# Optimization experiments

Measured on AMD Instinct MI355X. Metric: run time of the kernel, lower is better.

The kernel has to match this reference:

```python
import jax, jax.numpy as jnp
import numpy as np

B, Q, HID = 8, 8, 4096
H, KVH, D = 32, 8, 128
KV = 4096
ROPE_THETA = 10000.0


def rotate_half(x):
    x1, x2 = jnp.split(x, 2, axis=-1)
    return jnp.concatenate([-x2, x1], axis=-1)


def setup_inputs() -> dict:
    key = jax.random.key(0)
    ks = jax.random.split(key, 6)
    hidden_states = jax.random.normal(ks[0], (B, Q, HID), dtype=jnp.float32)
    position_ids = jnp.broadcast_to(jnp.arange(KV, dtype=jnp.int64), (B, KV))
    key_cache = jax.random.normal(ks[1], (B, KVH, KV, D), dtype=jnp.float32)
    value_cache = jax.random.normal(ks[2], (B, KVH, KV, D), dtype=jnp.float32)
    # mask: True -> blocked (-10000). Queries occupy last Q positions, causal.
    qpos = KV - Q + jnp.arange(Q)
    attention_mask = (jnp.arange(KV)[None, :] > qpos[:, None])[None, None]  # [1,1,Q,KV]
    attention_mask = jnp.broadcast_to(attention_mask, (B, 1, Q, KV))
    q_w = jax.random.normal(ks[3], (HID, HID), dtype=jnp.float32) * 0.02
    o_w = jax.random.normal(ks[4], (HID, HID), dtype=jnp.float32) * 0.02
    return {"hidden_states": hidden_states, "position_ids": position_ids,
            "key_cache": key_cache, "value_cache": value_cache,
            "attention_mask": attention_mask, "q_w": q_w, "o_w": o_w}


def reference(hidden_states, position_ids, key_cache, value_cache, attention_mask, q_w, o_w):
    # q projection: nn.Linear -> x @ W^T
    q = hidden_states @ q_w.T                       # [B,Q,HID]
    q = q.reshape(B, Q, H, D).transpose(0, 2, 1, 3)  # [B,H,Q,D]

    # rotary tables for kv_seq_len positions
    half = D // 2
    inv_freq = 1.0 / (ROPE_THETA ** (jnp.arange(0, half, dtype=jnp.float32) / half))
    t = jnp.arange(KV, dtype=jnp.float32)
    freqs = t[:, None] * inv_freq[None, :]           # [KV, D/2]
    emb = jnp.concatenate([freqs, freqs], axis=-1)   # [KV, D]
    cos_t, sin_t = jnp.cos(emb), jnp.sin(emb)

    # position_idx trick from the module: single effective rope position
    idx = jnp.argmax(position_ids.astype(jnp.int32), axis=1)[0]
    pid = jnp.take(position_ids, idx[None], axis=1)  # [B,1]
    cos = cos_t[pid][:, None]                        # [B,1,1,D]
    sin = sin_t[pid][:, None]
    q = q * cos + rotate_half(q) * sin               # [B,H,Q,D]

    # GQA attention without materializing repeat_kv (same math)
    G = H // KVH
    qg = q.reshape(B, KVH, G, Q, D)
    scores = jnp.einsum('bkgqd,bksd->bkgqs', qg, key_cache) / jnp.sqrt(jnp.float32(D))
    mask = attention_mask[:, :, None]                # [B,1,1,Q,KV]
    scores = jnp.where(mask, jnp.float32(-10000.0), scores)
    probs = jax.nn.softmax(scores.astype(jnp.float32), axis=-1).astype(q.dtype)
    out = jnp.einsum('bkgqs,bksd->bkgqd', probs, value_cache)  # [B,KVH,G,Q,D]
    out = out.reshape(B, H, Q, D).transpose(0, 2, 1, 3).reshape(B, Q, HID)
    return out @ o_w.T
```

## Files before the change

kernel.cpp:

```cpp
#include <hip/hip_runtime.h>
#include <math.h>

#define B_   8
#define Q_   8
#define HID  4096
#define NH   32
#define KVH_ 8
#define GQ   4
#define D_   128
#define KV_  4096
#define M_   64

#define OFF_COS   0
#define OFF_SIN   512
#define OFF_QROPE 1024
#define OFF_ATT   (OFF_QROPE + M_*HID)
#define OFF_OPART (OFF_ATT + M_*HID)
#define OFF_MPART (OFF_OPART + 64*8*32*128)
#define OFF_LPART (OFF_MPART + 64*8*32)
#define OFF_GPART (OFF_LPART + 64*8*32)

__global__ void prep_kernel(const int* __restrict__ pos, float* __restrict__ ws) {
    __shared__ int sv[256], si[256];
    __shared__ int s_idx;
    int t = threadIdx.x;
    int bv = -2147483647 - 1, bi = 0x7fffffff;
    for (int i = t; i < KV_; i += 256) {
        int v = pos[i];
        if (v > bv || (v == bv && i < bi)) { bv = v; bi = i; }
    }
    sv[t] = bv; si[t] = bi;
    __syncthreads();
    for (int off = 128; off > 0; off >>= 1) {
        if (t < off) {
            int v2 = sv[t + off], i2 = si[t + off];
            if (v2 > sv[t] || (v2 == sv[t] && i2 < si[t])) { sv[t] = v2; si[t] = i2; }
        }
        __syncthreads();
    }
    if (t == 0) s_idx = si[0];
    __syncthreads();
    int idx = s_idx;
    for (int u = t; u < B_ * 64; u += 256) {
        int b = u >> 6, d = u & 63;
        int pid = pos[b * KV_ + idx];
        float inv = __expf(-(float)d * (9.210340371976184f / 64.0f));
        float f = (float)pid * inv;
        ws[OFF_COS + u] = cosf(f);
        ws[OFF_SIN + u] = sinf(f);
    }
}

__global__ __launch_bounds__(128) void gemm_part(const float* __restrict__ A,
                                                 const float* __restrict__ W,
                                                 float* __restrict__ part) {
    __shared__ __align__(16) float As[2][32][68];
    __shared__ __align__(16) float Ws[2][32][68];
    int nc = blockIdx.x, kc = blockIdx.y;
    int t = threadIdx.x;
    int k0 = kc * 256;
    int n0 = nc * 64;
    int tx = t & 15, ty = t >> 4;
    int sr = t & 63, sq = t >> 6;

    const float* arow = A + (size_t)sr * HID + k0 + sq * 16;
    const float* wrow = W + (size_t)(n0 + sr) * HID + k0 + sq * 16;

    float acc[8][4];
    #pragma unroll
    for (int i = 0; i < 8; i++)
        #pragma unroll
        for (int j = 0; j < 4; j++) acc[i][j] = 0.f;

    #pragma unroll
    for (int c = 0; c < 4; ++c) {
        float4 av = *(const float4*)(arow + c * 4);
        float4 wv = *(const float4*)(wrow + c * 4);
        int q = sq * 4 + c;
        As[0][q*4+0][sr] = av.x; As[0][q*4+1][sr] = av.y;
        As[0][q*4+2][sr] = av.z; As[0][q*4+3][sr] = av.w;
        Ws[0][q*4+0][sr] = wv.x; Ws[0][q*4+1][sr] = wv.y;
        Ws[0][q*4+2][sr] = wv.z; Ws[0][q*4+3][sr] = wv.w;
    }
    __syncthreads();

    int cur = 0;
    for (int kt = 0; kt < 8; ++kt) {
        float4 ra[4], rw[4];
        if (kt < 7) {
            #pragma unroll
            for (int c = 0; c < 4; ++c) {
                ra[c] = *(const float4*)(arow + (kt + 1) * 32 + c * 4);
                rw[c] = *(const float4*)(wrow + (kt + 1) * 32 + c * 4);
            }
        }
        #pragma unroll
        for (int kk = 0; kk < 32; ++kk) {
            float4 a0 = *(const float4*)&As[cur][kk][ty * 8];
            float4 a1 = *(const float4*)&As[cur][kk][ty * 8 + 4];
            float4 w0 = *(const float4*)&Ws[cur][kk][tx * 4];
            float am[8] = {a0.x,a0.y,a0.z,a0.w,a1.x,a1.y,a1.z,a1.w};
            float wn[4] = {w0.x,w0.y,w0.z,w0.w};
            #pragma unroll
            for (int i = 0; i < 8; i++)
                #pragma unroll
                for (int j = 0; j < 4; j++)
                    acc[i][j] += am[i] * wn[j];
        }
        if (kt < 7) {
            int nb = cur ^ 1;
            #pragma unroll
            for (int c = 0; c < 4; ++c) {
                int q = sq * 4 + c;
                As[nb][q*4+0][sr] = ra[c].x; As[nb][q*4+1][sr] = ra[c].y;
                As[nb][q*4+2][sr] = ra[c].z; As[nb][q*4+3][sr] = ra[c].w;
                Ws[nb][q*4+0][sr] = rw[c].x; Ws[nb][q*4+1][sr] = rw[c].y;
                Ws[nb][q*4+2][sr] = rw[c].z; Ws[nb][q*4+3][sr] = rw[c].w;
            }
            __syncthreads();
            cur = nb;
        }
    }
    #pragma unroll
    for (int i = 0; i < 8; i++) {
        int m = ty * 8 + i;
        float* dst = part + ((size_t)kc * 64 + m) * HID + n0 + tx * 4;
        float4 v;
        v.x = acc[i][0]; v.y = acc[i][1]; v.z = acc[i][2]; v.w = acc[i][3];
        *(float4*)dst = v;
    }
}

__global__ void qrope_kernel(float* ws) {
    const float* part = ws + OFF_GPART;
    int blk = blockIdx.x;
    int b = blk >> 5, h = blk & 31;
    int t = threadIdx.x;
    int qq = t >> 5, dl = t & 31;
    int m = b * 8 + qq;
    int d0 = dl * 2;
    float x0 = 0, x1 = 0, y0 = 0, y1 = 0;
    const float* pbase = part + (size_t)m * HID + h * 128;
    #pragma unroll
    for (int kc = 0; kc < 16; ++kc) {
        const float* p = pbase + (size_t)kc * 64 * HID;
        x0 += p[d0];      x1 += p[d0 + 1];
        y0 += p[d0 + 64]; y1 += p[d0 + 65];
    }
    float c0 = ws[OFF_COS + b * 64 + d0], c1 = ws[OFF_COS + b * 64 + d0 + 1];
    float s0 = ws[OFF_SIN + b * 64 + d0], s1 = ws[OFF_SIN + b * 64 + d0 + 1];
    float* qr = ws + OFF_QROPE + ((size_t)(b * 32 + h)) * Q_ * D_ + (size_t)qq * D_;
    qr[d0]      = x0 * c0 - y0 * s0;
    qr[d0 + 1]  = x1 * c1 - y1 * s1;
    qr[d0 + 64] = y0 * c0 + x0 * s0;
    qr[d0 + 65] = y1 * c1 + x1 * s1;
}

#define CHUNK 512
#define TK 64
__global__ __launch_bounds__(256) void attn_kernel(const float* __restrict__ Kc,
                                                   const float* __restrict__ Vc,
                                                   float* __restrict__ ws) {
    __shared__ __align__(16) float qT[128][36];
    __shared__ __align__(16) float kT[128][68];
    __shared__ __align__(16) float pT[64][36];
    __shared__ float m_st[32], l_st[32], al_st[32];

    int c = blockIdx.x, kvh = blockIdx.y, b = blockIdx.z;
    int t = threadIdx.x;
    int pair = b * 8 + kvh;
    const float* qbase = ws + OFF_QROPE + (size_t)pair * 32 * 128;
    {
        int r = t & 31, qh = t >> 5;
        #pragma unroll
        for (int cq = 0; cq < 4; ++cq) {
            int dq = qh + cq * 8;
            float4 v = *(const float4*)(qbase + (size_t)r * 128 + dq * 4);
            qT[dq*4+0][r] = v.x; qT[dq*4+1][r] = v.y;
            qT[dq*4+2][r] = v.z; qT[dq*4+3][r] = v.w;
        }
    }
    if (t < 32) { m_st[t] = -INFINITY; l_st[t] = 0.f; }

    int st = t & 15;
    int dh = (t >> 4) & 1;
    int rt = t >> 5;
    int dt = t & 31;

    float o[4][4];
    #pragma unroll
    for (int i = 0; i < 4; i++)
        #pragma unroll
        for (int j = 0; j < 4; j++) o[i][j] = 0.f;

    const float* Kb = Kc + ((size_t)pair * KV_ + c * CHUNK) * D_;
    const float* Vb = Vc + ((size_t)pair * KV_ + c * CHUNK) * D_;
    const float scale = 0.08838834764831845f;

    for (int T = 0; T < CHUNK / TK; ++T) {
        int s0 = T * TK;
        __syncthreads();
        {
            int s = t >> 2, qr = t & 3;
            const float* kr = Kb + (size_t)(s0 + s) * D_ + qr * 4;
            #pragma unroll
            for (int cq = 0; cq < 8; ++cq) {
                float4 v = *(const float4*)(kr + cq * 16);
                int d = qr * 4 + cq * 16;
                kT[d+0][s] = v.x; kT[d+1][s] = v.y;
                kT[d+2][s] = v.z; kT[d+3][s] = v.w;
            }
        }
        __syncthreads();
        float S[4][4];
        #pragma unroll
        for (int i = 0; i < 4; i++)
            #pragma unroll
            for (int j = 0; j < 4; j++) S[i][j] = 0.f;
        int dbase = dh * 64;
        #pragma unroll 4
        for (int dd = 0; dd < 64; ++dd) {
            int d = dbase + dd;
            float4 q4 = *(const float4*)&qT[d][rt * 4];
            float4 k4 = *(const float4*)&kT[d][st * 4];
            float qa[4] = {q4.x, q4.y, q4.z, q4.w};
            float ka[4] = {k4.x, k4.y, k4.z, k4.w};
            #pragma unroll
            for (int i = 0; i < 4; i++)
            #pragma unroll
            for (int j = 0; j < 4; j++)
                S[i][j] += qa[i] * ka[j];
        }
        #pragma unroll
        for (int i = 0; i < 4; i++)
            #pragma unroll
            for (int j = 0; j < 4; j++)
                S[i][j] += __shfl_xor(S[i][j], 16, 64);
        int sabs_base = c * CHUNK + s0 + st * 4;
        #pragma unroll
        for (int i = 0; i < 4; i++) {
            int r = rt * 4 + i;
            int qq = r & 7;
            int qpos = KV_ - Q_ + qq;
            float v[4];
            float rmax = -INFINITY;
            #pragma unroll
            for (int j = 0; j < 4; j++) {
                int sa = sabs_base + j;
                float x = (sa > qpos) ? -10000.0f : S[i][j] * scale;
                v[j] = x;
                rmax = fmaxf(rmax, x);
            }
            for (int ml = 1; ml <= 8; ml <<= 1) rmax = fmaxf(rmax, __shfl_xor(rmax, ml, 64));
            float m_old = m_st[r];
            float m_new = fmaxf(m_old, rmax);
            float al = __expf(m_old - m_new);
            float ps = 0.f;
            #pragma unroll
            for (int j = 0; j < 4; j++) {
                float p = __expf(v[j] - m_new);
                if (dh == 0) pT[st * 4 + j][r] = p;
                ps += p;
            }
            for (int ml = 1; ml <= 8; ml <<= 1) ps += __shfl_xor(ps, ml, 64);
            if (st == 0 && dh == 0) {
                l_st[r] = l_st[r] * al + ps;
                m_st[r] = m_new;
                al_st[r] = al;
            }
        }
        __syncthreads();
        float al4[4];
        #pragma unroll
        for (int i = 0; i < 4; i++) al4[i] = al_st[rt * 4 + i];
        #pragma unroll
        for (int i = 0; i < 4; i++)
            #pragma unroll
            for (int j = 0; j < 4; j++) o[i][j] *= al4[i];
        const float* Vg = Vb + (size_t)s0 * D_ + dt * 4;
        #pragma unroll 8
        for (int s = 0; s < TK; ++s) {
            float4 p4 = *(const float4*)&pT[s][rt * 4];
            float4 v4 = *(const float4*)(Vg + (size_t)s * D_);
            float pp[4] = {p4.x, p4.y, p4.z, p4.w};
            float vv[4] = {v4.x, v4.y, v4.z, v4.w};
            #pragma unroll
            for (int i = 0; i < 4; i++)
            #pragma unroll
            for (int j = 0; j < 4; j++)
                o[i][j] += pp[i] * vv[j];
        }
    }
    float* opart = ws + OFF_OPART + ((size_t)pair * 8 + c) * 32 * 128;
    #pragma unroll
    for (int i = 0; i < 4; i++) {
        int r = rt * 4 + i;
        float* dst = opart + (size_t)r * 128 + dt * 4;
        float4 v;
        v.x = o[i][0]; v.y = o[i][1]; v.z = o[i][2]; v.w = o[i][3];
        *(float4*)dst = v;
    }
    __syncthreads();
    if (t < 32) {
        ws[OFF_MPART + ((size_t)pair * 8 + c) * 32 + t] = m_st[t];
        ws[OFF_LPART + ((size_t)pair * 8 + c) * 32 + t] = l_st[t];
    }
}

__global__ void combine_kernel(float* ws) {
    __shared__ float w_sh[8][32];
    int pair = blockIdx.x;
    int b = pair >> 3, kvh = pair & 7;
    int t = threadIdx.x;
    if (t < 32) {
        int r = t;
        float M = -INFINITY;
        float mv[8];
        #pragma unroll
        for (int cc = 0; cc < 8; ++cc) {
            mv[cc] = ws[OFF_MPART + ((size_t)pair * 8 + cc) * 32 + r];
            M = fmaxf(M, mv[cc]);
        }
        float L = 0.f;
        float e[8];
        #pragma unroll
        for (int cc = 0; cc < 8; ++cc) {
            e[cc] = __expf(mv[cc] - M);
            L += e[cc] * ws[OFF_LPART + ((size_t)pair * 8 + cc) * 32 + r];
        }
        float invL = 1.f / L;
        #pragma unroll
        for (int cc = 0; cc < 8; ++cc) w_sh[cc][r] = e[cc] * invL;
    }
    __syncthreads();
    const float* opart = ws + OFF_OPART + (size_t)pair * 8 * 32 * 128;
    float* aout = ws + OFF_ATT;
    for (int idx = t; idx < 32 * 128; idx += 256) {
        int r = idx >> 7, d = idx & 127;
        float acc = 0.f;
        #pragma unroll
        for (int cc = 0; cc < 8; ++cc)
            acc += w_sh[cc][r] * opart[((size_t)cc * 32 + r) * 128 + d];
        int g = r >> 3, qq = r & 7;
        aout[((size_t)(b * 8 + qq)) * HID + (kvh * 4 + g) * 128 + d] = acc;
    }
}

__global__ void oreduce_kernel(const float* __restrict__ part, float* __restrict__ out) {
    int idx = blockIdx.x * 256 + threadIdx.x;
    float4 acc = {0, 0, 0, 0};
    const float4* p = (const float4*)part;
    #pragma unroll
    for (int kc = 0; kc < 16; ++kc) {
        float4 v = p[(size_t)kc * 65536 + idx];
        acc.x += v.x; acc.y += v.y; acc.z += v.z; acc.w += v.w;
    }
    ((float4*)out)[idx] = acc;
}

extern "C" void kernel_launch(void* const* d_in, const int* in_sizes, int n_in,
                              void* d_out, int out_size, void* d_ws, size_t ws_size,
                              hipStream_t stream) {
    const float* hidden = (const float*)d_in[0];
    const int*   pos    = (const int*)d_in[1];
    const float* kcache = (const float*)d_in[2];
    const float* vcache = (const float*)d_in[3];
    const float* qw = (const float*)d_in[5];
    const float* ow = (const float*)d_in[6];
    float* ws  = (float*)d_ws;
    float* out = (float*)d_out;
    float* gpart = ws + OFF_GPART;

    prep_kernel<<<1, 256, 0, stream>>>(pos, ws);
    gemm_part<<<dim3(64, 16), 128, 0, stream>>>(hidden, qw, gpart);
    qrope_kernel<<<256, 256, 0, stream>>>(ws);
    attn_kernel<<<dim3(8, 8, 8), 256, 0, stream>>>(kcache, vcache, ws);
    combine_kernel<<<64, 256, 0, stream>>>(ws);
    gemm_part<<<dim3(64, 16), 128, 0, stream>>>(ws + OFF_ATT, ow, gpart);
    oreduce_kernel<<<256, 256, 0, stream>>>(gpart, out);
}
```

Before: 489.7 us.

## Use split-bf16 MFMA (3-pass) for the projection GEMMs

Replaces the FP32 FMA outer-product GEMM with MFMA 16x16x32 bf16 instructions. Each FP32 operand is split into hi and lo bf16 parts, and three products (hh, hl, lh) are accumulated to approximate FP32 accuracy. Shared-memory tiles are stored with an XOR swizzle, the block grows to 256 threads, and each K tile grows to 64. This moves the GEMMs onto matrix cores, at the cost of conversion work, extra shared memory, and a small loss of precision. The output stores are now scalar rather than float4.

```diff
diff --git a/kernel.cpp b/kernel.cpp
--- a/kernel.cpp
+++ b/kernel.cpp
@@ -19,6 +19,9 @@
 #define OFF_MPART (OFF_OPART + 64*8*32*128)
 #define OFF_LPART (OFF_MPART + 64*8*32)
 #define OFF_GPART (OFF_LPART + 64*8*32)
+
+typedef __attribute__((ext_vector_type(8))) short short8;
+typedef __attribute__((ext_vector_type(4))) float f32x4;
 
 __global__ void prep_kernel(const int* __restrict__ pos, float* __restrict__ ws) {
     __shared__ int sv[256], si[256];
@@ -51,83 +54,119 @@
     }
 }
 
-__global__ __launch_bounds__(128) void gemm_part(const float* __restrict__ A,
+__device__ __forceinline__ unsigned f2bf_rne(float x) {
+    unsigned u = __float_as_uint(x);
+    return (u + 0x7fffu + ((u >> 16) & 1u)) >> 16;
+}
+__device__ __forceinline__ float bf2f(unsigned h) { return __uint_as_float(h << 16); }
+
+__device__ __forceinline__ void cvt_store(unsigned short* __restrict__ ph,
+                                          unsigned short* __restrict__ pl,
+                                          int r, int q, const float4* v) {
+    unsigned hi[16], lo[16];
+    const float* f = (const float*)v;
+    #pragma unroll
+    for (int i = 0; i < 16; ++i) {
+        float x = f[i];
+        unsigned h = f2bf_rne(x);
+        hi[i] = h;
+        lo[i] = f2bf_rne(x - bf2f(h));
+    }
+    int s = r & 7;
+    #pragma unroll
+    for (int hf = 0; hf < 2; ++hf) {
+        int o = 2 * q + hf;
+        const unsigned* H = hi + hf * 8;
+        const unsigned* L = lo + hf * 8;
+        uint4 hv, lv;
+        hv.x = H[0] | (H[1] << 16); hv.y = H[2] | (H[3] << 16);
+        hv.z = H[4] | (H[5] << 16); hv.w = H[6] | (H[7] << 16);
+        lv.x = L[0] | (L[1] << 16); lv.y = L[2] | (L[3] << 16);
+        lv.z = L[4] | (L[5] << 16); lv.w = L[6] | (L[7] << 16);
+        *(uint4*)(ph + (size_t)r * 64 + ((o ^ s) * 8)) = hv;
+        *(uint4*)(pl + (size_t)r * 64 + ((o ^ s) * 8)) = lv;
+    }
+}
+
+__global__ __launch_bounds__(256) void gemm_part(const float* __restrict__ A,
                                                  const float* __restrict__ W,
                                                  float* __restrict__ part) {
-    __shared__ __align__(16) float As[2][32][68];
-    __shared__ __align__(16) float Ws[2][32][68];
+    __shared__ __align__(16) unsigned short AH[2][64][64];
+    __shared__ __align__(16) unsigned short AL[2][64][64];
+    __shared__ __align__(16) unsigned short WH[2][64][64];
+    __shared__ __align__(16) unsigned short WL[2][64][64];
+
     int nc = blockIdx.x, kc = blockIdx.y;
     int t = threadIdx.x;
-    int k0 = kc * 256;
-    int n0 = nc * 64;
-    int tx = t & 15, ty = t >> 4;
+    int k0 = kc * 256, n0 = nc * 64;
     int sr = t & 63, sq = t >> 6;
-
     const float* arow = A + (size_t)sr * HID + k0 + sq * 16;
     const float* wrow = W + (size_t)(n0 + sr) * HID + k0 + sq * 16;
 
-    float acc[8][4];
-    #pragma unroll
-    for (int i = 0; i < 8; i++)
-        #pragma unroll
-        for (int j = 0; j < 4; j++) acc[i][j] = 0.f;
-
-    #pragma unroll
-    for (int c = 0; c < 4; ++c) {
-        float4 av = *(const float4*)(arow + c * 4);
-        float4 wv = *(const float4*)(wrow + c * 4);
-        int q = sq * 4 + c;
-        As[0][q*4+0][sr] = av.x; As[0][q*4+1][sr] = av.y;
-        As[0][q*4+2][sr] = av.z; As[0][q*4+3][sr] = av.w;
-        Ws[0][q*4+0][sr] = wv.x; Ws[0][q*4+1][sr] = wv.y;
-        Ws[0][q*4+2][sr] = wv.z; Ws[0][q*4+3][sr] = wv.w;
+    f32x4 acc[4];
+    #pragma unroll
+    for (int ct = 0; ct < 4; ++ct) acc[ct] = (f32x4){0.f, 0.f, 0.f, 0.f};
+
+    {
+        float4 va[4], vw[4];
+        #pragma unroll
+        for (int c = 0; c < 4; ++c) {
+            va[c] = *(const float4*)(arow + c * 4);
+            vw[c] = *(const float4*)(wrow + c * 4);
+        }
+        cvt_store(&AH[0][0][0], &AL[0][0][0], sr, sq, va);
+        cvt_store(&WH[0][0][0], &WL[0][0][0], sr, sq, vw);
     }
     __syncthreads();
 
+    int w = t >> 6, l = t & 63;
+    int rA = 16 * w + (l & 15);
+    int sA = rA & 7;
+    int lq = l >> 4;
     int cur = 0;
-    for (int kt = 0; kt < 8; ++kt) {
-        float4 ra[4], rw[4];
-        if (kt < 7) {
+
+    for (int kt = 0; kt < 4; ++kt) {
+        float4 va[4], vw[4];
+        if (kt < 3) {
             #pragma unroll
             for (int c = 0; c < 4; ++c) {
-                ra[c] = *(const float4*)(arow + (kt + 1) * 32 + c * 4);
-                rw[c] = *(const float4*)(wrow + (kt + 1) * 32 + c * 4);
-            }
-        }
-        #pragma unroll
-        for (int kk = 0; kk < 32; ++kk) {
-            float4 a0 = *(const float4*)&As[cur][kk][ty * 8];
-            float4 a1 = *(const float4*)&As[cur][kk][ty * 8 + 4];
-            float4 w0 = *(const float4*)&Ws[cur][kk][tx * 4];
-            float am[8] = {a0.x,a0.y,a0.z,a0.w,a1.x,a1.y,a1.z,a1.w};
-            float wn[4] = {w0.x,w0.y,w0.z,w0.w};
-            #pragma unroll
-            for (int i = 0; i < 8; i++)
-                #pragma unroll
-                for (int j = 0; j < 4; j++)
-                    acc[i][j] += am[i] * wn[j];
-        }
-        if (kt < 7) {
+                va[c] = *(const float4*)(arow + (kt + 1) * 64 + c * 4);
+                vw[c] = *(const float4*)(wrow + (kt + 1) * 64 + c * 4);
+            }
+        }
+        #pragma unroll
+        for (int ks = 0; ks < 2; ++ks) {
+            int oct = ks * 4 + lq;
+            short8 ah = *(const short8*)&AH[cur][rA][(oct ^ sA) * 8];
+            short8 al = *(const short8*)&AL[cur][rA][(oct ^ sA) * 8];
+            #pragma unroll
+            for (int ct = 0; ct < 4; ++ct) {
+                int nB = ct * 16 + (l & 15);
+                int sB = nB & 7;
+                short8 bh = *(const short8*)&WH[cur][nB][(oct ^ sB) * 8];
+                short8 bl = *(const short8*)&WL[cur][nB][(oct ^ sB) * 8];
+                acc[ct] = __builtin_amdgcn_mfma_f32_16x16x32_bf16(ah, bh, acc[ct], 0, 0, 0);
+                acc[ct] = __builtin_amdgcn_mfma_f32_16x16x32_bf16(ah, bl, acc[ct], 0, 0, 0);
+                acc[ct] = __builtin_amdgcn_mfma_f32_16x16x32_bf16(al, bh, acc[ct], 0, 0, 0);
+            }
+        }
+        if (kt < 3) {
             int nb = cur ^ 1;
-            #pragma unroll
-            for (int c = 0; c < 4; ++c) {
-                int q = sq * 4 + c;
-                As[nb][q*4+0][sr] = ra[c].x; As[nb][q*4+1][sr] = ra[c].y;
-                As[nb][q*4+2][sr] = ra[c].z; As[nb][q*4+3][sr] = ra[c].w;
-                Ws[nb][q*4+0][sr] = rw[c].x; Ws[nb][q*4+1][sr] = rw[c].y;
-                Ws[nb][q*4+2][sr] = rw[c].z; Ws[nb][q*4+3][sr] = rw[c].w;
-            }
+            cvt_store(&AH[nb][0][0], &AL[nb][0][0], sr, sq, va);
+            cvt_store(&WH[nb][0][0], &WL[nb][0][0], sr, sq, vw);
             __syncthreads();
             cur = nb;
         }
     }
-    #pragma unroll
-    for (int i = 0; i < 8; i++) {
-        int m = ty * 8 + i;
-        float* dst = part + ((size_t)kc * 64 + m) * HID + n0 + tx * 4;
-        float4 v;
-        v.x = acc[i][0]; v.y = acc[i][1]; v.z = acc[i][2]; v.w = acc[i][3];
-        *(float4*)dst = v;
+
+    #pragma unroll
+    for (int ct = 0; ct < 4; ++ct) {
+        int n = n0 + ct * 16 + (l & 15);
+        #pragma unroll
+        for (int i = 0; i < 4; ++i) {
+            int m = 16 * w + lq * 4 + i;
+            part[((size_t)kc * 64 + m) * HID + n] = acc[ct][i];
+        }
     }
 }
 
@@ -372,10 +411,10 @@
     float* gpart = ws + OFF_GPART;
 
     prep_kernel<<<1, 256, 0, stream>>>(pos, ws);
-    gemm_part<<<dim3(64, 16), 128, 0, stream>>>(hidden, qw, gpart);
+    gemm_part<<<dim3(64, 16), 256, 0, stream>>>(hidden, qw, gpart);
     qrope_kernel<<<256, 256, 0, stream>>>(ws);
     attn_kernel<<<dim3(8, 8, 8), 256, 0, stream>>>(kcache, vcache, ws);
     combine_kernel<<<64, 256, 0, stream>>>(ws);
-    gemm_part<<<dim3(64, 16), 128, 0, stream>>>(ws + OFF_ATT, ow, gpart);
+    gemm_part<<<dim3(64, 16), 256, 0, stream>>>(ws + OFF_ATT, ow, gpart);
     oreduce_kernel<<<256, 256, 0, stream>>>(gpart, out);
 }
```

Result: faster. 461.2 us (-5.8%).
